# Kernel optimization log

Measured on AMD Instinct MI355X. Metric: run time of the kernel, lower is better.

The kernel has to match this reference:

```python
import jax, jax.numpy as jnp
import numpy as np

MARGIN = 0.3  # init kwarg, mode='norm'


def _pairwise_dist(X):
    # squared euclidean distances, then safe sqrt (matches euc_dist(X.t()).sqrt())
    sq = jnp.sum(X * X, axis=1)                      # [n]
    d2 = sq[:, None] + sq[None, :] - 2.0 * (X @ X.T)  # [n, n]
    d2 = jnp.maximum(d2, 0.0)
    # safe sqrt: avoid inf derivative at 0 (diagonal); forward value identical
    return jnp.where(d2 > 0.0, jnp.sqrt(jnp.where(d2 > 0.0, d2, 1.0)), 0.0)


def setup_inputs() -> dict:
    key = jax.random.key(0)
    kx, ky = jax.random.split(key)
    X = jax.random.normal(kx, (4096, 2048), dtype=jnp.float32)
    Y = jax.random.randint(ky, (4096,), 0, 128, dtype=jnp.int64)
    return {"X": X, "Y": Y}


def reference(X, Y):
    dist = _pairwise_dist(X)                         # [n, n]
    mask = Y[:, None] == Y[None, :]                  # same-identity mask [n, n]
    inf = jnp.array(jnp.inf, dtype=dist.dtype)
    # hardest positive per anchor: max over same-label entries
    dist_ap = jnp.max(jnp.where(mask, dist, -inf), axis=1)  # [n]
    # hardest negative per anchor: min over different-label entries
    dist_an = jnp.min(jnp.where(mask, inf, dist), axis=1)   # [n]
    # mode == 'norm': mean hinge
    return jnp.mean(jnp.maximum(dist_ap - dist_an + MARGIN, 0.0))
```

## Files before the change

### kernel.cpp

```cpp
#include <hip/hip_runtime.h>
#include <hip/hip_bf16.h>
#include <hip/hip_fp8.h>

typedef __attribute__((ext_vector_type(4))) int i32x4;
typedef __attribute__((ext_vector_type(8))) int i32x8;
typedef __attribute__((ext_vector_type(16))) float f32x16;

#define MARGIN 0.3f
#define BIGF 3.0e38f

__device__ __forceinline__ f32x16 mx_mfma(i32x8 a, i32x8 b, f32x16 c) {
    return __builtin_amdgcn_mfma_scale_f32_32x32x64_f8f6f4(
        a, b, c, 0 , 0 ,
        0, 127 , 0, 127 );
}

__device__ __forceinline__ i32x8 ld32(const unsigned char* p) {
    i32x4 lo = *(const i32x4*)p;
    i32x4 hi = *(const i32x4*)(p + 16);
    return __builtin_shufflevector(lo, hi, 0, 1, 2, 3, 4, 5, 6, 7);
}

__global__ __launch_bounds__(256) void convert_norm_kernel(
    const float* __restrict__ X, unsigned char* __restrict__ Xf,
    float* __restrict__ nrm, unsigned* __restrict__ ap,
    unsigned* __restrict__ an, unsigned* __restrict__ cnt, int K) {
    const int wave = threadIdx.x >> 6, lane = threadIdx.x & 63;
    const int row = blockIdx.x * 4 + wave;
    const float* xr = X + (size_t)row * K;
    const size_t pbase = ((size_t)(row >> 5)) << 16;
    const int rsub = row & 31;
    float s = 0.0f;
    for (int c = lane * 8; c < K; c += 64 * 8) {
        float4 v0 = *(const float4*)(xr + c);
        float4 v1 = *(const float4*)(xr + c + 4);
        float f[8] = {v0.x, v0.y, v0.z, v0.w, v1.x, v1.y, v1.z, v1.w};
        union { unsigned char b[8]; uint2 u; } p;
#pragma unroll
        for (int i = 0; i < 8; i++) {
            __hip_fp8_e4m3 q(f[i]);
            p.b[i] = q.__x;
            float d = (float)q;
            s += d * d;
        }
        const int lslot = rsub + (((c >> 5) & 1) << 5);
        unsigned char* dst = Xf + pbase + ((size_t)(c >> 6) << 11)
                             + (lslot << 5) + (c & 31);
        *(uint2*)dst = p.u;
    }
    for (int off = 32; off > 0; off >>= 1) s += __shfl_xor(s, off, 64);
    if (lane == 0) {
        nrm[row] = s;
        ap[row] = 0u;
        an[row] = 0x7F800000u;
        if (row == 0) *cnt = 0u;
    }
}

__global__ __launch_bounds__(256, 4) void gemm_reduce_kernel(
    const unsigned char* __restrict__ Xf, const float* __restrict__ nrm,
    const int* __restrict__ Y, unsigned* __restrict__ ap,
    unsigned* __restrict__ an, unsigned* __restrict__ cnt,
    float* __restrict__ out, int N, int K) {
    __shared__ int sYr[128], sYc[128];
    __shared__ float sNr[128], sNc[128];
    __shared__ float redmax[4][64], redmin[4][64];
    __shared__ float lsum[4];
    __shared__ unsigned s_done;

    const int tid = threadIdx.x;
    const int wave = tid >> 6;
    const int lane = tid & 63;
    const int m = lane & 31;
    const int h = lane >> 5;
    const int wr = wave >> 1;
    const int wc = wave & 1;

    const int NB = N >> 7;
    const int rowBase = (blockIdx.x >> 5) * 128;
    const int colBase = (blockIdx.x & (NB - 1)) * 128;

    if (tid < 128) {
        sYr[tid] = Y[rowBase + tid];
        sNr[tid] = nrm[rowBase + tid];
    } else {
        int t = tid - 128;
        sYc[t] = Y[colBase + t];
        sNc[t] = nrm[colBase + t];
    }
    __syncthreads();

    f32x16 acc[2][2];
#pragma unroll
    for (int si = 0; si < 2; si++)
#pragma unroll
        for (int sj = 0; sj < 2; sj++)
#pragma unroll
            for (int rr = 0; rr < 16; rr++) acc[si][sj][rr] = 0.0f;

    const unsigned char* a0 =
        Xf + (((size_t)(rowBase >> 5) + wr * 2) << 16) + lane * 32;
    const unsigned char* a1 = a0 + 65536;
    const unsigned char* b0 =
        Xf + (((size_t)(colBase >> 5) + wc * 2) << 16) + lane * 32;
    const unsigned char* b1 = b0 + 65536;

    const int nt = K >> 6;
#pragma unroll 4
    for (int t = 0; t < nt; t++) {
        const size_t off = (size_t)t << 11;
        i32x8 af0 = ld32(a0 + off);
        i32x8 af1 = ld32(a1 + off);
        i32x8 bf0 = ld32(b0 + off);
        i32x8 bf1 = ld32(b1 + off);
        acc[0][0] = mx_mfma(af0, bf0, acc[0][0]);
        acc[0][1] = mx_mfma(af0, bf1, acc[0][1]);
        acc[1][0] = mx_mfma(af1, bf0, acc[1][0]);
        acc[1][1] = mx_mfma(af1, bf1, acc[1][1]);
    }

#pragma unroll
    for (int si = 0; si < 2; si++)
#pragma unroll
        for (int reg = 0; reg < 16; reg++) {
            const int row64 = si * 32 + (reg & 3) + 8 * (reg >> 2) + 4 * h;
            const int rIdx = wr * 64 + row64;
            const int yr = sYr[rIdx];
            const float nr = sNr[rIdx];
            float dp = -1.0f, dn = BIGF;
#pragma unroll
            for (int sj = 0; sj < 2; sj++) {
                const int cIdx = wc * 64 + sj * 32 + m;
                float d2 = nr + sNc[cIdx] - 2.0f * acc[si][sj][reg];
                float d = sqrtf(fmaxf(d2, 0.0f));
                bool same = (yr == sYc[cIdx]);
                dp = fmaxf(dp, same ? d : -1.0f);
                dn = fminf(dn, same ? BIGF : d);
            }
            for (int off = 1; off < 32; off <<= 1) {
                dp = fmaxf(dp, __shfl_xor(dp, off, 64));
                dn = fminf(dn, __shfl_xor(dn, off, 64));
            }
            if (m == 0) {
                redmax[wave][row64] = dp;
                redmin[wave][row64] = dn;
            }
        }
    __syncthreads();

    if (tid < 128) {
        const int wr2 = tid >> 6, r64 = tid & 63;
        float mx = fmaxf(redmax[wr2 * 2][r64], redmax[wr2 * 2 + 1][r64]);
        float mn = fminf(redmin[wr2 * 2][r64], redmin[wr2 * 2 + 1][r64]);
        atomicMax(&ap[rowBase + tid], __float_as_uint(fmaxf(mx, 0.0f)));
        atomicMin(&an[rowBase + tid], __float_as_uint(mn));
    }

    __syncthreads();
    if (tid == 0) {
        __threadfence();
        s_done = atomicAdd(cnt, 1u);
    }
    __syncthreads();
    if (s_done == gridDim.x - 1) {
        __threadfence();
        float s = 0.0f;
        for (int i = tid; i < N; i += 256) {
            unsigned ua = __hip_atomic_load(&ap[i], __ATOMIC_RELAXED,
                                            __HIP_MEMORY_SCOPE_AGENT);
            unsigned ub = __hip_atomic_load(&an[i], __ATOMIC_RELAXED,
                                            __HIP_MEMORY_SCOPE_AGENT);
            s += fmaxf(__uint_as_float(ua) - __uint_as_float(ub) + MARGIN, 0.0f);
        }
        for (int off = 32; off > 0; off >>= 1) s += __shfl_xor(s, off, 64);
        if (lane == 0) lsum[wave] = s;
        __syncthreads();
        if (tid == 0)
            out[0] = (lsum[0] + lsum[1] + lsum[2] + lsum[3]) / (float)N;
    }
}

extern "C" void kernel_launch(void* const* d_in, const int* in_sizes, int n_in,
                              void* d_out, int out_size, void* d_ws, size_t ws_size,
                              hipStream_t stream) {
    const float* X = (const float*)d_in[0];
    const int* Y = (const int*)d_in[1];
    float* out = (float*)d_out;
    const int N = in_sizes[1];
    const int K = in_sizes[0] / N;

    char* ws = (char*)d_ws;
    unsigned char* Xf = (unsigned char*)ws;
    float* nrm = (float*)(ws + (size_t)N * K);
    unsigned* ap = (unsigned*)((char*)nrm + (size_t)N * 4);
    unsigned* an = (unsigned*)((char*)ap + (size_t)N * 4);
    unsigned* cnt = (unsigned*)((char*)an + (size_t)N * 4);

    convert_norm_kernel<<<N / 4, 256, 0, stream>>>(X, Xf, nrm, ap, an, cnt, K);
    const int NB = N / 128;
    gemm_reduce_kernel<<<NB * NB, 256, 0, stream>>>(Xf, nrm, Y, ap, an, cnt,
                                                    out, N, K);
}
```

Before: 132.9 us.

## Enlarge GEMM block tile to 256x128 with register double-buffered fragment loads

Each block now covers 256 rows by 128 columns, and each wave owns a 64x128 sub-tile with 2x4 MFMA accumulators instead of 2x2. Fragment loads are double-buffered in registers so the next k-step's loads are in flight while the current MFMAs run. The shared-memory cross-wave reduction is replaced by per-wave atomics to global memory. The aim is more operand reuse per byte loaded and better hiding of load latency. The costs are higher register pressure (launch bounds lowered to 2 blocks per SIMD), half as many blocks, and more global atomics. Grid indexing now hardcodes 32 column blocks, so it assumes N=4096.

```diff
diff --git a/kernel.cpp b/kernel.cpp
--- a/kernel.cpp
+++ b/kernel.cpp
@@ -57,14 +57,13 @@
     }
 }
 
-__global__ __launch_bounds__(256, 4) void gemm_reduce_kernel(
+__global__ __launch_bounds__(256, 2) void gemm_reduce_kernel(
     const unsigned char* __restrict__ Xf, const float* __restrict__ nrm,
     const int* __restrict__ Y, unsigned* __restrict__ ap,
     unsigned* __restrict__ an, unsigned* __restrict__ cnt,
     float* __restrict__ out, int N, int K) {
-    __shared__ int sYr[128], sYc[128];
-    __shared__ float sNr[128], sNc[128];
-    __shared__ float redmax[4][64], redmin[4][64];
+    __shared__ int sYr[256], sYc[128];
+    __shared__ float sNr[256], sNc[128];
     __shared__ float lsum[4];
     __shared__ unsigned s_done;
 
@@ -73,64 +72,84 @@
     const int lane = tid & 63;
     const int m = lane & 31;
     const int h = lane >> 5;
-    const int wr = wave >> 1;
-    const int wc = wave & 1;
-
-    const int NB = N >> 7;
-    const int rowBase = (blockIdx.x >> 5) * 128;
-    const int colBase = (blockIdx.x & (NB - 1)) * 128;
-
-    if (tid < 128) {
+
+    const int rowBase = (blockIdx.x >> 5) << 8;
+    const int colBase = (blockIdx.x & 31) << 7;
+
+    if (tid < 256) {
         sYr[tid] = Y[rowBase + tid];
         sNr[tid] = nrm[rowBase + tid];
-    } else {
-        int t = tid - 128;
-        sYc[t] = Y[colBase + t];
-        sNc[t] = nrm[colBase + t];
-    }
+    }
+    if (tid < 128) {
+        sYc[tid] = Y[colBase + tid];
+        sNc[tid] = nrm[colBase + tid];
+    }
+
+    f32x16 acc[2][4];
+#pragma unroll
+    for (int si = 0; si < 2; si++)
+#pragma unroll
+        for (int sj = 0; sj < 4; sj++)
+#pragma unroll
+            for (int rr = 0; rr < 16; rr++) acc[si][sj][rr] = 0.0f;
+
+    const unsigned char* pa[2];
+    const unsigned char* pb[4];
+#pragma unroll
+    for (int si = 0; si < 2; si++)
+        pa[si] = Xf + (((size_t)(rowBase >> 5) + wave * 2 + si) << 16) + lane * 32;
+#pragma unroll
+    for (int sj = 0; sj < 4; sj++)
+        pb[sj] = Xf + (((size_t)(colBase >> 5) + sj) << 16) + lane * 32;
+
+    i32x8 A0[2], B0[4], A1[2], B1[4];
+
+#define LD(Ab, Bb, t)                                                   \
+    do {                                                                \
+        const size_t _o = (size_t)(t) << 11;                            \
+        _Pragma("unroll") for (int _i = 0; _i < 2; _i++)                \
+            Ab[_i] = ld32(pa[_i] + _o);                                 \
+        _Pragma("unroll") for (int _j = 0; _j < 4; _j++)                \
+            Bb[_j] = ld32(pb[_j] + _o);                                 \
+    } while (0)
+
+#define MM(Ab, Bb)                                                      \
+    do {                                                                \
+        _Pragma("unroll") for (int _i = 0; _i < 2; _i++)                \
+            _Pragma("unroll") for (int _j = 0; _j < 4; _j++)            \
+                acc[_i][_j] = mx_mfma(Ab[_i], Bb[_j], acc[_i][_j]);     \
+    } while (0)
+
+    const int nt = K >> 6;
+    LD(A0, B0, 0);
+    int t = 0;
+    for (; t + 2 < nt; t += 2) {
+        LD(A1, B1, t + 1);
+        MM(A0, B0);
+        LD(A0, B0, t + 2);
+        MM(A1, B1);
+    }
+    LD(A1, B1, t + 1);
+    MM(A0, B0);
+    MM(A1, B1);
+
+#undef LD
+#undef MM
+
     __syncthreads();
-
-    f32x16 acc[2][2];
-#pragma unroll
-    for (int si = 0; si < 2; si++)
-#pragma unroll
-        for (int sj = 0; sj < 2; sj++)
-#pragma unroll
-            for (int rr = 0; rr < 16; rr++) acc[si][sj][rr] = 0.0f;
-
-    const unsigned char* a0 =
-        Xf + (((size_t)(rowBase >> 5) + wr * 2) << 16) + lane * 32;
-    const unsigned char* a1 = a0 + 65536;
-    const unsigned char* b0 =
-        Xf + (((size_t)(colBase >> 5) + wc * 2) << 16) + lane * 32;
-    const unsigned char* b1 = b0 + 65536;
-
-    const int nt = K >> 6;
-#pragma unroll 4
-    for (int t = 0; t < nt; t++) {
-        const size_t off = (size_t)t << 11;
-        i32x8 af0 = ld32(a0 + off);
-        i32x8 af1 = ld32(a1 + off);
-        i32x8 bf0 = ld32(b0 + off);
-        i32x8 bf1 = ld32(b1 + off);
-        acc[0][0] = mx_mfma(af0, bf0, acc[0][0]);
-        acc[0][1] = mx_mfma(af0, bf1, acc[0][1]);
-        acc[1][0] = mx_mfma(af1, bf0, acc[1][0]);
-        acc[1][1] = mx_mfma(af1, bf1, acc[1][1]);
-    }
 
 #pragma unroll
     for (int si = 0; si < 2; si++)
 #pragma unroll
         for (int reg = 0; reg < 16; reg++) {
             const int row64 = si * 32 + (reg & 3) + 8 * (reg >> 2) + 4 * h;
-            const int rIdx = wr * 64 + row64;
+            const int rIdx = wave * 64 + row64;
             const int yr = sYr[rIdx];
             const float nr = sNr[rIdx];
             float dp = -1.0f, dn = BIGF;
 #pragma unroll
-            for (int sj = 0; sj < 2; sj++) {
-                const int cIdx = wc * 64 + sj * 32 + m;
+            for (int sj = 0; sj < 4; sj++) {
+                const int cIdx = sj * 32 + m;
                 float d2 = nr + sNc[cIdx] - 2.0f * acc[si][sj][reg];
                 float d = sqrtf(fmaxf(d2, 0.0f));
                 bool same = (yr == sYc[cIdx]);
@@ -142,19 +161,10 @@
                 dn = fminf(dn, __shfl_xor(dn, off, 64));
             }
             if (m == 0) {
-                redmax[wave][row64] = dp;
-                redmin[wave][row64] = dn;
+                atomicMax(&ap[rowBase + rIdx], __float_as_uint(fmaxf(dp, 0.0f)));
+                atomicMin(&an[rowBase + rIdx], __float_as_uint(dn));
             }
         }
-    __syncthreads();
-
-    if (tid < 128) {
-        const int wr2 = tid >> 6, r64 = tid & 63;
-        float mx = fmaxf(redmax[wr2 * 2][r64], redmax[wr2 * 2 + 1][r64]);
-        float mn = fminf(redmin[wr2 * 2][r64], redmin[wr2 * 2 + 1][r64]);
-        atomicMax(&ap[rowBase + tid], __float_as_uint(fmaxf(mx, 0.0f)));
-        atomicMin(&an[rowBase + tid], __float_as_uint(mn));
-    }
 
     __syncthreads();
     if (tid == 0) {
@@ -197,7 +207,7 @@
     unsigned* cnt = (unsigned*)((char*)an + (size_t)N * 4);
 
     convert_norm_kernel<<<N / 4, 256, 0, stream>>>(X, Xf, nrm, ap, an, cnt, K);
-    const int NB = N / 128;
-    gemm_reduce_kernel<<<NB * NB, 256, 0, stream>>>(Xf, nrm, Y, ap, an, cnt,
-                                                    out, N, K);
-}
+    const int NBr = N / 256, NBc = N / 128;
+    gemm_reduce_kernel<<<NBr * NBc, 256, 0, stream>>>(Xf, nrm, Y, ap, an, cnt,
+                                                      out, N, K);
+}
```

New measurement: 128.6 us. 1.03x faster.

## Exploit distance symmetry by computing only upper-triangular tiles with row and column reductions

Applied to the files above, without the earlier changes.

The GEMM-reduce grid now covers only upper-triangular 128x128 tiles (ti <= tj) and cuts the tile count roughly in half. Each tile also does a column-wise max/min and updates ap/an for the column rows, so the symmetric distance matrix is used once for both sides. The costs are a serial loop to map block index to tile, extra shared-memory reductions, and twice as many atomics per tile. Diagonal tiles write to the same rows from both passes, which is still correct for max and min.

```diff
diff --git a/kernel.cpp b/kernel.cpp
--- a/kernel.cpp
+++ b/kernel.cpp
@@ -65,6 +65,7 @@
     __shared__ int sYr[128], sYc[128];
     __shared__ float sNr[128], sNc[128];
     __shared__ float redmax[4][64], redmin[4][64];
+    __shared__ float cmax[4][64], cmin[4][64];
     __shared__ float lsum[4];
     __shared__ unsigned s_done;
 
@@ -77,18 +78,20 @@
     const int wc = wave & 1;
 
     const int NB = N >> 7;
-    const int rowBase = (blockIdx.x >> 5) * 128;
-    const int colBase = (blockIdx.x & (NB - 1)) * 128;
+    int bi = blockIdx.x, ti = 0;
+    while (bi >= NB - ti) { bi -= NB - ti; ti++; }
+    const int tj = ti + bi;
+    const int rowBase = ti << 7;
+    const int colBase = tj << 7;
 
     if (tid < 128) {
         sYr[tid] = Y[rowBase + tid];
         sNr[tid] = nrm[rowBase + tid];
     } else {
-        int t = tid - 128;
-        sYc[t] = Y[colBase + t];
-        sNc[t] = nrm[colBase + t];
-    }
-    __syncthreads();
+        const int t0 = tid - 128;
+        sYc[t0] = Y[colBase + t0];
+        sNc[t0] = nrm[colBase + t0];
+    }
 
     f32x16 acc[2][2];
 #pragma unroll
@@ -98,27 +101,33 @@
 #pragma unroll
             for (int rr = 0; rr < 16; rr++) acc[si][sj][rr] = 0.0f;
 
-    const unsigned char* a0 =
-        Xf + (((size_t)(rowBase >> 5) + wr * 2) << 16) + lane * 32;
-    const unsigned char* a1 = a0 + 65536;
-    const unsigned char* b0 =
-        Xf + (((size_t)(colBase >> 5) + wc * 2) << 16) + lane * 32;
-    const unsigned char* b1 = b0 + 65536;
+    const unsigned char* pa[2];
+    const unsigned char* pb[2];
+#pragma unroll
+    for (int si = 0; si < 2; si++)
+        pa[si] = Xf + (((size_t)(rowBase >> 5) + wr * 2 + si) << 16) + lane * 32;
+#pragma unroll
+    for (int sj = 0; sj < 2; sj++)
+        pb[sj] = Xf + (((size_t)(colBase >> 5) + wc * 2 + sj) << 16) + lane * 32;
 
     const int nt = K >> 6;
 #pragma unroll 4
     for (int t = 0; t < nt; t++) {
         const size_t off = (size_t)t << 11;
-        i32x8 af0 = ld32(a0 + off);
-        i32x8 af1 = ld32(a1 + off);
-        i32x8 bf0 = ld32(b0 + off);
-        i32x8 bf1 = ld32(b1 + off);
-        acc[0][0] = mx_mfma(af0, bf0, acc[0][0]);
-        acc[0][1] = mx_mfma(af0, bf1, acc[0][1]);
-        acc[1][0] = mx_mfma(af1, bf0, acc[1][0]);
-        acc[1][1] = mx_mfma(af1, bf1, acc[1][1]);
-    }
-
+        i32x8 a0 = ld32(pa[0] + off);
+        i32x8 a1 = ld32(pa[1] + off);
+        i32x8 b0 = ld32(pb[0] + off);
+        i32x8 b1 = ld32(pb[1] + off);
+        acc[0][0] = mx_mfma(a0, b0, acc[0][0]);
+        acc[0][1] = mx_mfma(a0, b1, acc[0][1]);
+        acc[1][0] = mx_mfma(a1, b0, acc[1][0]);
+        acc[1][1] = mx_mfma(a1, b1, acc[1][1]);
+    }
+
+    __syncthreads();
+
+    float cdp[2] = {-1.0f, -1.0f};
+    float cdn[2] = {BIGF, BIGF};
 #pragma unroll
     for (int si = 0; si < 2; si++)
 #pragma unroll
@@ -134,8 +143,12 @@
                 float d2 = nr + sNc[cIdx] - 2.0f * acc[si][sj][reg];
                 float d = sqrtf(fmaxf(d2, 0.0f));
                 bool same = (yr == sYc[cIdx]);
-                dp = fmaxf(dp, same ? d : -1.0f);
-                dn = fminf(dn, same ? BIGF : d);
+                float vp = same ? d : -1.0f;
+                float vn = same ? BIGF : d;
+                dp = fmaxf(dp, vp);
+                dn = fminf(dn, vn);
+                cdp[sj] = fmaxf(cdp[sj], vp);
+                cdn[sj] = fminf(cdn[sj], vn);
             }
             for (int off = 1; off < 32; off <<= 1) {
                 dp = fmaxf(dp, __shfl_xor(dp, off, 64));
@@ -146,6 +159,15 @@
                 redmin[wave][row64] = dn;
             }
         }
+#pragma unroll
+    for (int sj = 0; sj < 2; sj++) {
+        cdp[sj] = fmaxf(cdp[sj], __shfl_xor(cdp[sj], 32, 64));
+        cdn[sj] = fminf(cdn[sj], __shfl_xor(cdn[sj], 32, 64));
+        if (h == 0) {
+            cmax[wave][sj * 32 + m] = cdp[sj];
+            cmin[wave][sj * 32 + m] = cdn[sj];
+        }
+    }
     __syncthreads();
 
     if (tid < 128) {
@@ -154,6 +176,13 @@
         float mn = fminf(redmin[wr2 * 2][r64], redmin[wr2 * 2 + 1][r64]);
         atomicMax(&ap[rowBase + tid], __float_as_uint(fmaxf(mx, 0.0f)));
         atomicMin(&an[rowBase + tid], __float_as_uint(mn));
+    } else {
+        const int t0 = tid - 128;
+        const int wc2 = t0 >> 6, c64 = t0 & 63;
+        float mx = fmaxf(cmax[wc2][c64], cmax[2 + wc2][c64]);
+        float mn = fminf(cmin[wc2][c64], cmin[2 + wc2][c64]);
+        atomicMax(&ap[colBase + t0], __float_as_uint(fmaxf(mx, 0.0f)));
+        atomicMin(&an[colBase + t0], __float_as_uint(mn));
     }
 
     __syncthreads();
@@ -198,6 +227,7 @@
 
     convert_norm_kernel<<<N / 4, 256, 0, stream>>>(X, Xf, nrm, ap, an, cnt, K);
     const int NB = N / 128;
-    gemm_reduce_kernel<<<NB * NB, 256, 0, stream>>>(Xf, nrm, Y, ap, an, cnt,
-                                                    out, N, K);
-}
+    const int ntri = NB * (NB + 1) / 2;
+    gemm_reduce_kernel<<<ntri, 256, 0, stream>>>(Xf, nrm, Y, ap, an, cnt,
+                                                 out, N, K);
+}
```

Measured after the change: 133.4 us. No clear change (+0.4%).
